# Kernel optimization log

Hardware: AMD Instinct MI355X
Metric: run time of the kernel (lower is better)

Reference implementation:

```python
import jax, jax.numpy as jnp
import numpy as np

N = 100000
E = 1000000
D = 32          # numerical_dim
HID = 64        # hidden_dim
OUT = 1         # output_dim
REL = 4 * D     # relation feature dim
EPS = 1e-8


def setup_inputs() -> dict:
    key = jax.random.key(0)
    k_x, k_e, k_w1, k_b1, k_w2, k_b2 = jax.random.split(key, 6)
    x = jax.random.uniform(k_x, (N, D), dtype=jnp.float32)
    edge_index = jax.random.randint(k_e, (2, E), 0, N, dtype=jnp.int64)
    # Linear params (PyTorch convention: W [out, in], y = x @ W.T + b)
    lim1 = 1.0 / np.sqrt(REL)
    W1 = jax.random.uniform(k_w1, (HID, REL), minval=-lim1, maxval=lim1, dtype=jnp.float32)
    b1 = jax.random.uniform(k_b1, (HID,), minval=-lim1, maxval=lim1, dtype=jnp.float32)
    lim2 = 1.0 / np.sqrt(HID)
    W2 = jax.random.uniform(k_w2, (OUT, HID), minval=-lim2, maxval=lim2, dtype=jnp.float32)
    b2 = jax.random.uniform(k_b2, (OUT,), minval=-lim2, maxval=lim2, dtype=jnp.float32)
    return {"x": x, "edge_index": edge_index, "W1": W1, "b1": b1, "W2": W2, "b2": b2}


def _relation_features(x_i, x_j):
    ratio = x_i / (x_j + EPS)
    log_ratio = jnp.log(x_i + EPS) - jnp.log(x_j + EPS)
    abs_diff = jnp.abs(x_i - x_j)
    rel_diff = abs_diff / (jnp.maximum(x_i, x_j) + EPS)
    return jnp.concatenate([ratio, log_ratio, abs_diff, rel_diff], axis=-1)  # [E, 4D]


def reference(x, edge_index, W1, b1, W2, b2):
    src, dst = edge_index[0], edge_index[1]
    x_i = x[src]                      # [E, D] gather source node feats
    x_j = x[dst]                      # [E, D] gather target node feats
    rel = _relation_features(x_i, x_j)  # [E, 4D]
    h = jax.nn.relu(rel @ W1.T + b1)    # [E, HID]
    edge_bias = (h @ W2.T + b2).squeeze(-1)  # [E]
    return edge_bias
```

## Files before the change

kernel.cpp:

```cpp
#include <hip/hip_runtime.h>


#define DD    32
#define HID   64
#define RELF  128
#define EPSF  1e-8f

typedef short  bf16x8 __attribute__((ext_vector_type(8)));
typedef float  f32x4  __attribute__((ext_vector_type(4)));

union U8 { unsigned u[4]; bf16x8 v; };

static __device__ __forceinline__ unsigned pk_tr(float lo, float hi) {
    return __builtin_amdgcn_perm(__builtin_bit_cast(unsigned, hi),
                                 __builtin_bit_cast(unsigned, lo), 0x07060302u);
}
static __device__ __forceinline__ unsigned rne_bits(float f) {
    unsigned u = __builtin_bit_cast(unsigned, f);
    return u + 0x7fffu + ((u >> 16) & 1u);
}
static __device__ __forceinline__ unsigned pk_rne(float lo, float hi) {
    return __builtin_amdgcn_perm(rne_bits(hi), rne_bits(lo), 0x07060302u);
}
static __device__ __forceinline__ float hi_f32(float f) {
    return __builtin_bit_cast(float, __builtin_bit_cast(unsigned, f) & 0xffff0000u);
}

__global__ __launch_bounds__(256)
void prep_logx(const float* __restrict__ x, unsigned* __restrict__ lx, int nq)
{
    int i = blockIdx.x * blockDim.x + threadIdx.x;
    if (i >= nq) return;
    float4 v = ((const float4*)x)[i];
    uint2 o;
    o.x = pk_rne(__logf(v.x + EPSF), __logf(v.y + EPSF));
    o.y = pk_rne(__logf(v.z + EPSF), __logf(v.w + EPSF));
    ((uint2*)lx)[i] = o;
}

template <int PRE>
__global__ __launch_bounds__(256, 2)
void edge_bias_mfma(const float* __restrict__ x,
                    const int*   __restrict__ ei,
                    const float* __restrict__ W1,
                    const float* __restrict__ b1,
                    const float* __restrict__ W2,
                    const float* __restrict__ b2,
                    const short* __restrict__ lx,
                    float* __restrict__ out,
                    int E)
{
    const int lane = threadIdx.x & 63;
    const int wave = (blockIdx.x * blockDim.x + threadIdx.x) >> 6;
    const int nwv  = (gridDim.x * blockDim.x) >> 6;
    const int c = lane & 15;
    const int q = lane >> 4;

    bf16x8 W0h[4], W0l[4], WL[4], WLn[4], WA[4], WDm[4];
    #pragma unroll
    for (int nt = 0; nt < 4; ++nt) {
        const float* wr = W1 + (nt * 16 + c) * RELF + q * 8;
        U8 h, l, tt;
        #pragma unroll
        for (int p = 0; p < 4; ++p) {
            float w0 = wr[2 * p], w1 = wr[2 * p + 1];
            h.u[p] = pk_tr(w0, w1);
            l.u[p] = pk_rne(w0 - hi_f32(w0), w1 - hi_f32(w1));
        }
        W0h[nt] = h.v; W0l[nt] = l.v;
        #pragma unroll
        for (int p = 0; p < 4; ++p)
            tt.u[p] = pk_rne(wr[32 + 2 * p], wr[32 + 2 * p + 1]);
        WL[nt] = tt.v;
        #pragma unroll
        for (int p = 0; p < 4; ++p) tt.u[p] ^= 0x80008000u;
        WLn[nt] = tt.v;
        #pragma unroll
        for (int p = 0; p < 4; ++p)
            tt.u[p] = pk_rne(wr[64 + 2 * p], wr[64 + 2 * p + 1]);
        WA[nt] = tt.v;
        #pragma unroll
        for (int p = 0; p < 4; ++p)
            tt.u[p] = pk_rne(wr[96 + 2 * p], wr[96 + 2 * p + 1]);
        WDm[nt] = tt.v;
    }
    float b1v[4], w2v[4];
    #pragma unroll
    for (int nt = 0; nt < 4; ++nt) {
        b1v[nt] = b1[nt * 16 + c];
        w2v[nt] = W2[nt * 16 + c];
    }
    const float b2s = b2[0];

    const int ntiles = (E + 15) >> 4;
    int t = wave;
    if (t >= ntiles) return;

    float4 xi0C, xi1C, xj0C, xj1C;
    bf16x8 LiC, LjC;
    int srcN, dstN;

    {
        int em = (t << 4) + c; if (em > E - 1) em = E - 1;
        int s = ei[em], d = ei[E + em];
        const float* pi = x + (long)s * DD + q * 8;
        const float* pj = x + (long)d * DD + q * 8;
        xi0C = ((const float4*)pi)[0]; xi1C = ((const float4*)pi)[1];
        xj0C = ((const float4*)pj)[0]; xj1C = ((const float4*)pj)[1];
        if (PRE) {
            LiC = *(const bf16x8*)(lx + (long)s * DD + q * 8);
            LjC = *(const bf16x8*)(lx + (long)d * DD + q * 8);
        }
    }
    {
        int t1 = t + nwv; if (t1 >= ntiles) t1 = t;
        int em = (t1 << 4) + c; if (em > E - 1) em = E - 1;
        srcN = ei[em]; dstN = ei[E + em];
    }

    for (; t < ntiles; t += nwv) {
        float4 xi0N, xi1N, xj0N, xj1N;
        bf16x8 LiN, LjN;
        {
            const float* pi = x + (long)srcN * DD + q * 8;
            const float* pj = x + (long)dstN * DD + q * 8;
            xi0N = ((const float4*)pi)[0]; xi1N = ((const float4*)pi)[1];
            xj0N = ((const float4*)pj)[0]; xj1N = ((const float4*)pj)[1];
            if (PRE) {
                LiN = *(const bf16x8*)(lx + (long)srcN * DD + q * 8);
                LjN = *(const bf16x8*)(lx + (long)dstN * DD + q * 8);
            }
        }
        int srcN2, dstN2;
        {
            int t2 = t + 2 * nwv; if (t2 >= ntiles) t2 = t;
            int em = (t2 << 4) + c; if (em > E - 1) em = E - 1;
            srcN2 = ei[em]; dstN2 = ei[E + em];
        }

        const int e0 = t << 4;
        float xiv[8] = {xi0C.x, xi0C.y, xi0C.z, xi0C.w, xi1C.x, xi1C.y, xi1C.z, xi1C.w};
        float xjv[8] = {xj0C.x, xj0C.y, xj0C.z, xj0C.w, xj1C.x, xj1C.y, xj1C.z, xj1C.w};

        bf16x8 aLi, aLj;
        if constexpr (PRE) {
            aLi = LiC; aLj = LjC;
        } else {
            U8 ti, tj;
            #pragma unroll
            for (int p = 0; p < 4; ++p) {
                ti.u[p] = pk_rne(__logf(xiv[2*p] + EPSF), __logf(xiv[2*p+1] + EPSF));
                tj.u[p] = pk_rne(__logf(xjv[2*p] + EPSF), __logf(xjv[2*p+1] + EPSF));
            }
            aLi = ti.v; aLj = tj.v;
        }

        U8 R, Rl, Aa, Dd;
        #pragma unroll
        for (int p = 0; p < 4; ++p) {
            float a0 = xiv[2*p], a1 = xiv[2*p+1];
            float c0 = xjv[2*p], c1 = xjv[2*p+1];
            float r0 = a0 * __builtin_amdgcn_rcpf(c0 + EPSF);
            float r1 = a1 * __builtin_amdgcn_rcpf(c1 + EPSF);
            float d0 = fabsf(a0 - c0), d1 = fabsf(a1 - c1);
            float g0 = d0 * __builtin_amdgcn_rcpf(fmaxf(a0, c0) + EPSF);
            float g1 = d1 * __builtin_amdgcn_rcpf(fmaxf(a1, c1) + EPSF);
            R.u[p]  = pk_tr(r0, r1);
            Rl.u[p] = pk_tr(r0 - hi_f32(r0), r1 - hi_f32(r1));
            Aa.u[p] = pk_tr(d0, d1);
            Dd.u[p] = pk_tr(g0, g1);
        }

        f32x4 acc[4];
        #pragma unroll
        for (int nt = 0; nt < 4; ++nt) {
            acc[nt][0] = b1v[nt]; acc[nt][1] = b1v[nt];
            acc[nt][2] = b1v[nt]; acc[nt][3] = b1v[nt];
        }
        #pragma unroll
        for (int nt = 0; nt < 4; ++nt) {
            acc[nt] = __builtin_amdgcn_mfma_f32_16x16x32_bf16(R.v,  W0h[nt], acc[nt], 0, 0, 0);
            acc[nt] = __builtin_amdgcn_mfma_f32_16x16x32_bf16(Rl.v, W0h[nt], acc[nt], 0, 0, 0);
            acc[nt] = __builtin_amdgcn_mfma_f32_16x16x32_bf16(R.v,  W0l[nt], acc[nt], 0, 0, 0);
            acc[nt] = __builtin_amdgcn_mfma_f32_16x16x32_bf16(aLi,  WL[nt],  acc[nt], 0, 0, 0);
            acc[nt] = __builtin_amdgcn_mfma_f32_16x16x32_bf16(aLj,  WLn[nt], acc[nt], 0, 0, 0);
            acc[nt] = __builtin_amdgcn_mfma_f32_16x16x32_bf16(Aa.v, WA[nt],  acc[nt], 0, 0, 0);
            acc[nt] = __builtin_amdgcn_mfma_f32_16x16x32_bf16(Dd.v, WDm[nt], acc[nt], 0, 0, 0);
        }

        float p[4];
        #pragma unroll
        for (int r = 0; r < 4; ++r) {
            float pp = 0.f;
            #pragma unroll
            for (int nt = 0; nt < 4; ++nt)
                pp = fmaf(fmaxf(acc[nt][r], 0.f), w2v[nt], pp);
            pp += __shfl_xor(pp, 1);
            pp += __shfl_xor(pp, 2);
            pp += __shfl_xor(pp, 4);
            pp += __shfl_xor(pp, 8);
            p[r] = pp;
        }
        if (c < 4) {
            const int e = e0 + q * 4 + c;
            if (e < E) {
                float v = (c == 0) ? p[0] : (c == 1) ? p[1] : (c == 2) ? p[2] : p[3];
                out[e] = v + b2s;
            }
        }

        xi0C = xi0N; xi1C = xi1N; xj0C = xj0N; xj1C = xj1N;
        LiC = LiN;  LjC = LjN;
        srcN = srcN2; dstN = dstN2;
    }
}

extern "C" void kernel_launch(void* const* d_in, const int* in_sizes, int n_in,
                              void* d_out, int out_size, void* d_ws, size_t ws_size,
                              hipStream_t stream)
{
    const float* x   = (const float*)d_in[0];
    const int*   ei  = (const int*)  d_in[1];
    const float* W1  = (const float*)d_in[2];
    const float* b1  = (const float*)d_in[3];
    const float* W2  = (const float*)d_in[4];
    const float* b2  = (const float*)d_in[5];
    float* out = (float*)d_out;

    const int E  = out_size;
    const int Nd = in_sizes[0];
    short* lx = (short*)d_ws;

    const bool pre = ws_size >= (size_t)Nd * sizeof(short) && (Nd % 4) == 0;
    if (pre) {
        const int nq = Nd / 4;
        prep_logx<<<(nq + 255) / 256, 256, 0, stream>>>(x, (unsigned*)lx, nq);
        edge_bias_mfma<1><<<1024, 256, 0, stream>>>(x, ei, W1, b1, W2, b2, lx, out, E);
    } else {
        edge_bias_mfma<0><<<1024, 256, 0, stream>>>(x, ei, W1, b1, W2, b2, lx, out, E);
    }
}
```

Before: 144.9 us.

## Compute log-ratio inline, drop log precompute kernel, merge log MFMAs, double grid

Removes the separate prep_logx kernel and its workspace log table, and computes log(xi)-log(xj) inline per edge in fp32 before a single bf16 packing. This replaces two MFMAs per tile (log_i with W, log_j with negated W) with one and removes the two extra bf16x8 gathers per edge. The grid goes from 1024 to 2048 blocks. The cost is more transcendental ALU work per edge, since each log is now recomputed for every edge that touches a node instead of once per node.

```diff
diff --git a/kernel.cpp b/kernel.cpp
--- a/kernel.cpp
+++ b/kernel.cpp
@@ -26,19 +26,6 @@
     return __builtin_bit_cast(float, __builtin_bit_cast(unsigned, f) & 0xffff0000u);
 }
 
-__global__ __launch_bounds__(256)
-void prep_logx(const float* __restrict__ x, unsigned* __restrict__ lx, int nq)
-{
-    int i = blockIdx.x * blockDim.x + threadIdx.x;
-    if (i >= nq) return;
-    float4 v = ((const float4*)x)[i];
-    uint2 o;
-    o.x = pk_rne(__logf(v.x + EPSF), __logf(v.y + EPSF));
-    o.y = pk_rne(__logf(v.z + EPSF), __logf(v.w + EPSF));
-    ((uint2*)lx)[i] = o;
-}
-
-template <int PRE>
 __global__ __launch_bounds__(256, 2)
 void edge_bias_mfma(const float* __restrict__ x,
                     const int*   __restrict__ ei,
@@ -46,7 +33,6 @@
                     const float* __restrict__ b1,
                     const float* __restrict__ W2,
                     const float* __restrict__ b2,
-                    const short* __restrict__ lx,
                     float* __restrict__ out,
                     int E)
 {
@@ -56,7 +42,7 @@
     const int c = lane & 15;
     const int q = lane >> 4;
 
-    bf16x8 W0h[4], W0l[4], WL[4], WLn[4], WA[4], WDm[4];
+    bf16x8 W0h[4], W0l[4], WLf[4], WAf[4], WDf[4];
     #pragma unroll
     for (int nt = 0; nt < 4; ++nt) {
         const float* wr = W1 + (nt * 16 + c) * RELF + q * 8;
@@ -71,18 +57,15 @@
         #pragma unroll
         for (int p = 0; p < 4; ++p)
             tt.u[p] = pk_rne(wr[32 + 2 * p], wr[32 + 2 * p + 1]);
-        WL[nt] = tt.v;
-        #pragma unroll
-        for (int p = 0; p < 4; ++p) tt.u[p] ^= 0x80008000u;
-        WLn[nt] = tt.v;
+        WLf[nt] = tt.v;
         #pragma unroll
         for (int p = 0; p < 4; ++p)
             tt.u[p] = pk_rne(wr[64 + 2 * p], wr[64 + 2 * p + 1]);
-        WA[nt] = tt.v;
+        WAf[nt] = tt.v;
         #pragma unroll
         for (int p = 0; p < 4; ++p)
             tt.u[p] = pk_rne(wr[96 + 2 * p], wr[96 + 2 * p + 1]);
-        WDm[nt] = tt.v;
+        WDf[nt] = tt.v;
     }
     float b1v[4], w2v[4];
     #pragma unroll
@@ -97,7 +80,6 @@
     if (t >= ntiles) return;
 
     float4 xi0C, xi1C, xj0C, xj1C;
-    bf16x8 LiC, LjC;
     int srcN, dstN;
 
     {
@@ -107,10 +89,6 @@
         const float* pj = x + (long)d * DD + q * 8;
         xi0C = ((const float4*)pi)[0]; xi1C = ((const float4*)pi)[1];
         xj0C = ((const float4*)pj)[0]; xj1C = ((const float4*)pj)[1];
-        if (PRE) {
-            LiC = *(const bf16x8*)(lx + (long)s * DD + q * 8);
-            LjC = *(const bf16x8*)(lx + (long)d * DD + q * 8);
-        }
     }
     {
         int t1 = t + nwv; if (t1 >= ntiles) t1 = t;
@@ -120,16 +98,11 @@
 
     for (; t < ntiles; t += nwv) {
         float4 xi0N, xi1N, xj0N, xj1N;
-        bf16x8 LiN, LjN;
         {
             const float* pi = x + (long)srcN * DD + q * 8;
             const float* pj = x + (long)dstN * DD + q * 8;
             xi0N = ((const float4*)pi)[0]; xi1N = ((const float4*)pi)[1];
             xj0N = ((const float4*)pj)[0]; xj1N = ((const float4*)pj)[1];
-            if (PRE) {
-                LiN = *(const bf16x8*)(lx + (long)srcN * DD + q * 8);
-                LjN = *(const bf16x8*)(lx + (long)dstN * DD + q * 8);
-            }
         }
         int srcN2, dstN2;
         {
@@ -142,29 +115,19 @@
         float xiv[8] = {xi0C.x, xi0C.y, xi0C.z, xi0C.w, xi1C.x, xi1C.y, xi1C.z, xi1C.w};
         float xjv[8] = {xj0C.x, xj0C.y, xj0C.z, xj0C.w, xj1C.x, xj1C.y, xj1C.z, xj1C.w};
 
-        bf16x8 aLi, aLj;
-        if constexpr (PRE) {
-            aLi = LiC; aLj = LjC;
-        } else {
-            U8 ti, tj;
-            #pragma unroll
-            for (int p = 0; p < 4; ++p) {
-                ti.u[p] = pk_rne(__logf(xiv[2*p] + EPSF), __logf(xiv[2*p+1] + EPSF));
-                tj.u[p] = pk_rne(__logf(xjv[2*p] + EPSF), __logf(xjv[2*p+1] + EPSF));
-            }
-            aLi = ti.v; aLj = tj.v;
-        }
-
-        U8 R, Rl, Aa, Dd;
+        U8 R, Rl, Aa, Dd, L;
         #pragma unroll
         for (int p = 0; p < 4; ++p) {
             float a0 = xiv[2*p], a1 = xiv[2*p+1];
             float c0 = xjv[2*p], c1 = xjv[2*p+1];
+            float l0 = __logf(a0 + EPSF) - __logf(c0 + EPSF);
+            float l1 = __logf(a1 + EPSF) - __logf(c1 + EPSF);
             float r0 = a0 * __builtin_amdgcn_rcpf(c0 + EPSF);
             float r1 = a1 * __builtin_amdgcn_rcpf(c1 + EPSF);
             float d0 = fabsf(a0 - c0), d1 = fabsf(a1 - c1);
             float g0 = d0 * __builtin_amdgcn_rcpf(fmaxf(a0, c0) + EPSF);
             float g1 = d1 * __builtin_amdgcn_rcpf(fmaxf(a1, c1) + EPSF);
+            L.u[p]  = pk_tr(l0, l1);
             R.u[p]  = pk_tr(r0, r1);
             Rl.u[p] = pk_tr(r0 - hi_f32(r0), r1 - hi_f32(r1));
             Aa.u[p] = pk_tr(d0, d1);
@@ -182,10 +145,9 @@
             acc[nt] = __builtin_amdgcn_mfma_f32_16x16x32_bf16(R.v,  W0h[nt], acc[nt], 0, 0, 0);
             acc[nt] = __builtin_amdgcn_mfma_f32_16x16x32_bf16(Rl.v, W0h[nt], acc[nt], 0, 0, 0);
             acc[nt] = __builtin_amdgcn_mfma_f32_16x16x32_bf16(R.v,  W0l[nt], acc[nt], 0, 0, 0);
-            acc[nt] = __builtin_amdgcn_mfma_f32_16x16x32_bf16(aLi,  WL[nt],  acc[nt], 0, 0, 0);
-            acc[nt] = __builtin_amdgcn_mfma_f32_16x16x32_bf16(aLj,  WLn[nt], acc[nt], 0, 0, 0);
-            acc[nt] = __builtin_amdgcn_mfma_f32_16x16x32_bf16(Aa.v, WA[nt],  acc[nt], 0, 0, 0);
-            acc[nt] = __builtin_amdgcn_mfma_f32_16x16x32_bf16(Dd.v, WDm[nt], acc[nt], 0, 0, 0);
+            acc[nt] = __builtin_amdgcn_mfma_f32_16x16x32_bf16(L.v,  WLf[nt], acc[nt], 0, 0, 0);
+            acc[nt] = __builtin_amdgcn_mfma_f32_16x16x32_bf16(Aa.v, WAf[nt], acc[nt], 0, 0, 0);
+            acc[nt] = __builtin_amdgcn_mfma_f32_16x16x32_bf16(Dd.v, WDf[nt], acc[nt], 0, 0, 0);
         }
 
         float p[4];
@@ -210,7 +172,6 @@
         }
 
         xi0C = xi0N; xi1C = xi1N; xj0C = xj0N; xj1C = xj1N;
-        LiC = LiN;  LjC = LjN;
         srcN = srcN2; dstN = dstN2;
     }
 }
@@ -227,16 +188,6 @@
     const float* b2  = (const float*)d_in[5];
     float* out = (float*)d_out;
 
-    const int E  = out_size;
-    const int Nd = in_sizes[0];
-    short* lx = (short*)d_ws;
-
-    const bool pre = ws_size >= (size_t)Nd * sizeof(short) && (Nd % 4) == 0;
-    if (pre) {
-        const int nq = Nd / 4;
-        prep_logx<<<(nq + 255) / 256, 256, 0, stream>>>(x, (unsigned*)lx, nq);
-        edge_bias_mfma<1><<<1024, 256, 0, stream>>>(x, ei, W1, b1, W2, b2, lx, out, E);
-    } else {
-        edge_bias_mfma<0><<<1024, 256, 0, stream>>>(x, ei, W1, b1, W2, b2, lx, out, E);
-    }
+    const int E = out_size;
+    edge_bias_mfma<<<2048, 256, 0, stream>>>(x, ei, W1, b1, W2, b2, out, E);
 }
```

After: 160.2 us. 1.11x slower.
